# Optimization experiments

Measured on AMD Instinct MI355X. Metric: run time of the kernel, lower is better.

The kernel has to match this reference:

```python
import jax, jax.numpy as jnp
import numpy as np

VOCAB, EMB, OUT = 32000, 1024, 10
B, S = 64, 512

def setup_inputs() -> dict:
    key = jax.random.key(0)
    k1, k2, k3, k4, k5, k6, k7 = jax.random.split(key, 7)
    x = jax.random.randint(k1, (B, S), 0, VOCAB)
    label = jax.random.randint(k2, (B,), 0, OUT)
    emb_table = jax.random.normal(k3, (VOCAB, EMB), dtype=jnp.float32) * 0.02
    W = jax.random.normal(k4, (EMB, EMB), dtype=jnp.float32) / np.sqrt(EMB)
    b = jax.random.normal(k5, (EMB,), dtype=jnp.float32) * 0.01
    Wc = jax.random.normal(k6, (OUT, EMB), dtype=jnp.float32) / np.sqrt(EMB)
    bc = jax.random.normal(k7, (OUT,), dtype=jnp.float32) * 0.01
    return {"x": x, "label": label, "emb_table": emb_table, "W": W, "b": b, "Wc": Wc, "bc": bc}

def reference(x, label, emb_table, W, b, Wc, bc):
    # embedding lookup: (B, S, EMB)
    emb = emb_table[x]
    # affine recurrence h_i = W @ (h_{i-1} + x_i) + b, h_{-1} = 0
    def step(h, xi):
        h = (h + xi) @ W.T + b  # (B, EMB)
        return h, h
    h0 = jnp.zeros((emb.shape[0], emb.shape[2]), dtype=emb.dtype)
    _, hs = jax.lax.scan(step, h0, jnp.swapaxes(emb, 0, 1))  # hs: (S, B, EMB)
    result = jnp.swapaxes(hs, 0, 1)  # (B, S, EMB)
    pred = result @ Wc.T + bc  # (B, S, OUT)
    pred_mean = jnp.mean(pred, axis=1)  # (B, OUT)
    # cross entropy (mean reduction)
    logp = jax.nn.log_softmax(pred_mean, axis=-1)
    loss = -jnp.mean(jnp.take_along_axis(logp, label[:, None], axis=-1))
    return loss
```

## Files before the change

kernel.cpp:

```cpp
#include <hip/hip_runtime.h>

#define OFF_C    0L
#define OFF_CS   11272192L
#define OFF_WP   11354112L
#define OFF_PRED 11446272L
#define OFF_PART 11446912L
#define OFF_U16  11774592L
#define UQAH 0L
#define UQAL 1048576L
#define UQATH 2097152L
#define UQATL 3145728L
#define UQBH 4194304L
#define UQBL 5242880L
#define UQBTH 6291456L
#define UQBTL 7340032L
#define URH  8388608L
#define CSA  1409024L
#define CSB  2621440L

typedef unsigned short u16;
typedef unsigned int u32;
typedef u16 us8 __attribute__((ext_vector_type(8)));
typedef short s8v __attribute__((ext_vector_type(8)));
typedef float f4v __attribute__((ext_vector_type(4)));

__device__ __forceinline__ u16 f2b(float f) {
    u32 u = __float_as_uint(f);
    return (u16)((u + 0x7fffu + ((u >> 16) & 1u)) >> 16);
}
__device__ __forceinline__ float b2f(u16 h) {
    return __uint_as_float((u32)h << 16);
}

__global__ __launch_bounds__(256) void split_w(
    const float* __restrict__ W, u16* __restrict__ Qh, u16* __restrict__ Ql,
    u16* __restrict__ QTh, u16* __restrict__ QTl)
{
    __shared__ u32 T[64][65];
    const int tid = threadIdx.x;
    const int r = tid >> 2, c0 = (tid & 3) << 4;
    alignas(16) u16 h[16], l[16];
    const size_t src = (size_t)(blockIdx.y * 64 + r) * 1024 + blockIdx.x * 64 + c0;
    #pragma unroll
    for (int q = 0; q < 4; q++) {
        float4 v = *(const float4*)(W + src + q * 4);
        float vv[4] = {v.x, v.y, v.z, v.w};
        #pragma unroll
        for (int i = 0; i < 4; i++) {
            u16 hh = f2b(vv[i]);
            u16 ll = f2b(vv[i] - b2f(hh));
            h[q * 4 + i] = hh; l[q * 4 + i] = ll;
            T[c0 + q * 4 + i][r] = ((u32)ll << 16) | hh;
        }
    }
    *(us8*)(Qh + src) = *(const us8*)&h[0];
    *(us8*)(Qh + src + 8) = *(const us8*)&h[8];
    *(us8*)(Ql + src) = *(const us8*)&l[0];
    *(us8*)(Ql + src + 8) = *(const us8*)&l[8];
    __syncthreads();
    alignas(16) u16 th[16], tl[16];
    #pragma unroll
    for (int i = 0; i < 16; i++) {
        u32 v = T[r][c0 + i];
        th[i] = (u16)(v & 0xffffu); tl[i] = (u16)(v >> 16);
    }
    const size_t dst = (size_t)(blockIdx.x * 64 + r) * 1024 + blockIdx.y * 64 + c0;
    *(us8*)(QTh + dst) = *(const us8*)&th[0];
    *(us8*)(QTh + dst + 8) = *(const us8*)&th[8];
    *(us8*)(QTl + dst) = *(const us8*)&tl[0];
    *(us8*)(QTl + dst + 8) = *(const us8*)&tl[8];
}

__global__ __launch_bounds__(256) void d0_k(
    const float* __restrict__ Wc, const float* __restrict__ W, u16* __restrict__ Rh)
{
    __shared__ float WcS[10240];
    __shared__ float red[8][332];
    const int tid = threadIdx.x;
    const int d = tid & 31, kz = tid >> 5;
    const int dbase = blockIdx.x << 5;
    for (int i = tid; i < 2560; i += 256)
        ((float4*)WcS)[i] = ((const float4*)Wc)[i];
    __syncthreads();
    float acc[10] = {};
    const int k0 = kz << 7;
    for (int k = 0; k < 128; k++) {
        float w = W[(size_t)(k0 + k) * 1024 + dbase + d];
        #pragma unroll
        for (int o = 0; o < 10; o++)
            acc[o] = fmaf(WcS[o * 1024 + k0 + k], w, acc[o]);
    }
    #pragma unroll
    for (int o = 0; o < 10; o++) red[kz][o * 32 + d] = acc[o];
    __syncthreads();
    for (int t = tid; t < 320; t += 256) {
        float s = 0.f;
        #pragma unroll
        for (int z = 0; z < 8; z++) s += red[z][t];
        Rh[(size_t)(t >> 5) * 1024 + dbase + (t & 31)] = f2b(s);
    }
}

__global__ __launch_bounds__(256) void gemm_mfma(
    const u16* __restrict__ Ah_g, const u16* __restrict__ Al_g,
    const u16* __restrict__ Rh_g,
    const u16* __restrict__ BTh_g, const u16* __restrict__ BTl_g,
    float* __restrict__ C, int a1M, int a2M, int kc, long cS)
{
    const int M = a1M + a2M;
    __shared__ alignas(16) u16 Ash[4][129][8], Asl[4][129][8];
    __shared__ alignas(16) u16 Bsh[4][129][8], Bsl[4][129][8];
    const int tid = threadIdx.x;
    const int bn = blockIdx.x << 7, bm = blockIdx.y << 7;
    const int kstart = blockIdx.z * kc, kend = kstart + kc;
    const int lane = tid & 63, wid = tid >> 6;
    const int wm = (wid & 1) << 6, wn = (wid >> 1) << 6;
    const int lrow = lane & 15, kq = lane >> 4;
    const int srow = tid >> 1;
    const int skq = (tid & 1) << 1;
    const int sk = skq << 3;

    const u16* pBh = BTh_g + (size_t)(bn + srow) * 1024;
    const u16* pBl = BTl_g + (size_t)(bn + srow) * 1024;

    f4v acc[4][4];
    #pragma unroll
    for (int i = 0; i < 4; i++)
        #pragma unroll
        for (int j = 0; j < 4; j++) acc[i][j] = 0.f;

    if (bm < a1M) {
        const u16* pAh = Ah_g + (size_t)(bm + srow) * 1024;
        const u16* pAl = Al_g + (size_t)(bm + srow) * 1024;
        us8 ah0, ah1, al0, al1, bh0, bh1, bl0, bl1;
        auto loadstep = [&](int k) {
            ah0 = *(const us8*)(pAh + k + sk); ah1 = *(const us8*)(pAh + k + sk + 8);
            al0 = *(const us8*)(pAl + k + sk); al1 = *(const us8*)(pAl + k + sk + 8);
            bh0 = *(const us8*)(pBh + k + sk); bh1 = *(const us8*)(pBh + k + sk + 8);
            bl0 = *(const us8*)(pBl + k + sk); bl1 = *(const us8*)(pBl + k + sk + 8);
        };
        loadstep(kstart);
        for (int k0 = kstart; k0 < kend; k0 += 32) {
            *(us8*)&Ash[skq][srow][0] = ah0;
            *(us8*)&Ash[skq + 1][srow][0] = ah1;
            *(us8*)&Asl[skq][srow][0] = al0;
            *(us8*)&Asl[skq + 1][srow][0] = al1;
            *(us8*)&Bsh[skq][srow][0] = bh0;
            *(us8*)&Bsh[skq + 1][srow][0] = bh1;
            *(us8*)&Bsl[skq][srow][0] = bl0;
            *(us8*)&Bsl[skq + 1][srow][0] = bl1;
            __syncthreads();
            if (k0 + 32 < kend) loadstep(k0 + 32);
            s8v afh[4], afl[4], bfh[4], bfl[4];
            #pragma unroll
            for (int i = 0; i < 4; i++) {
                afh[i] = *(const s8v*)&Ash[kq][wm + (i << 4) + lrow][0];
                afl[i] = *(const s8v*)&Asl[kq][wm + (i << 4) + lrow][0];
                bfh[i] = *(const s8v*)&Bsh[kq][wn + (i << 4) + lrow][0];
                bfl[i] = *(const s8v*)&Bsl[kq][wn + (i << 4) + lrow][0];
            }
            #pragma unroll
            for (int mi = 0; mi < 4; mi++)
                #pragma unroll
                for (int ni = 0; ni < 4; ni++) {
                    acc[mi][ni] = __builtin_amdgcn_mfma_f32_16x16x32_bf16(
                        afh[mi], bfh[ni], acc[mi][ni], 0, 0, 0);
                    acc[mi][ni] = __builtin_amdgcn_mfma_f32_16x16x32_bf16(
                        afl[mi], bfh[ni], acc[mi][ni], 0, 0, 0);
                    acc[mi][ni] = __builtin_amdgcn_mfma_f32_16x16x32_bf16(
                        afh[mi], bfl[ni], acc[mi][ni], 0, 0, 0);
                }
            __syncthreads();
        }
    } else {
        const int rr = bm + srow - a1M;
        const bool aval = (rr < a2M);
        const u16* pAh = Rh_g + (size_t)(aval ? rr : 0) * 1024;
        us8 ah0, ah1, bh0, bh1, bl0, bl1;
        auto loadstep = [&](int k) {
            if (aval) {
                ah0 = *(const us8*)(pAh + k + sk); ah1 = *(const us8*)(pAh + k + sk + 8);
            } else { ah0 = 0; ah1 = 0; }
            bh0 = *(const us8*)(pBh + k + sk); bh1 = *(const us8*)(pBh + k + sk + 8);
            bl0 = *(const us8*)(pBl + k + sk); bl1 = *(const us8*)(pBl + k + sk + 8);
        };
        loadstep(kstart);
        for (int k0 = kstart; k0 < kend; k0 += 32) {
            *(us8*)&Ash[skq][srow][0] = ah0;
            *(us8*)&Ash[skq + 1][srow][0] = ah1;
            *(us8*)&Bsh[skq][srow][0] = bh0;
            *(us8*)&Bsh[skq + 1][srow][0] = bh1;
            *(us8*)&Bsl[skq][srow][0] = bl0;
            *(us8*)&Bsl[skq + 1][srow][0] = bl1;
            __syncthreads();
            if (k0 + 32 < kend) loadstep(k0 + 32);
            s8v afh[4], bfh[4], bfl[4];
            #pragma unroll
            for (int i = 0; i < 4; i++) {
                afh[i] = *(const s8v*)&Ash[kq][wm + (i << 4) + lrow][0];
                bfh[i] = *(const s8v*)&Bsh[kq][wn + (i << 4) + lrow][0];
                bfl[i] = *(const s8v*)&Bsl[kq][wn + (i << 4) + lrow][0];
            }
            #pragma unroll
            for (int mi = 0; mi < 4; mi++)
                #pragma unroll
                for (int ni = 0; ni < 4; ni++) {
                    acc[mi][ni] = __builtin_amdgcn_mfma_f32_16x16x32_bf16(
                        afh[mi], bfh[ni], acc[mi][ni], 0, 0, 0);
                    acc[mi][ni] = __builtin_amdgcn_mfma_f32_16x16x32_bf16(
                        afh[mi], bfl[ni], acc[mi][ni], 0, 0, 0);
                }
            __syncthreads();
        }
    }
    float* Cz = C + (size_t)blockIdx.z * cS;
    #pragma unroll
    for (int mi = 0; mi < 4; mi++)
        #pragma unroll
        for (int i = 0; i < 4; i++) {
            const int gr = bm + wm + (mi << 4) + (kq << 2) + i;
            if (gr >= M) continue;
            #pragma unroll
            for (int ni = 0; ni < 4; ni++)
                Cz[(size_t)gr * 1024 + bn + wn + (ni << 4) + lrow] = acc[mi][ni][i];
        }
}

__global__ __launch_bounds__(256) void combine(
    const float* __restrict__ C, int zsplit, long cS, int a1M, int a2M, int M,
    u16* __restrict__ Qh, u16* __restrict__ Ql,
    u16* __restrict__ QTh, u16* __restrict__ QTl,
    u16* __restrict__ Rh)
{
    __shared__ u32 T[64][65];
    const int tid = threadIdx.x;
    const int r = tid >> 2, c0 = (tid & 3) << 4;
    const int row0 = blockIdx.y << 6, col0 = blockIdx.x << 6;
    const int gr = row0 + r;
    const bool isQ = (row0 < a1M);
    alignas(16) u16 h[16], l[16];
    #pragma unroll
    for (int q = 0; q < 4; q++) {
        float4 v = make_float4(0.f, 0.f, 0.f, 0.f);
        if (gr < M) {
            const float* p = C + (size_t)gr * 1024 + col0 + c0 + q * 4;
            v = *(const float4*)p;
            for (int z = 1; z < zsplit; z++) {
                float4 t2 = *(const float4*)(p + (size_t)z * cS);
                v.x += t2.x; v.y += t2.y; v.z += t2.z; v.w += t2.w;
            }
        }
        float vv[4] = {v.x, v.y, v.z, v.w};
        #pragma unroll
        for (int i = 0; i < 4; i++) {
            u16 hh = f2b(vv[i]);
            u16 ll = f2b(vv[i] - b2f(hh));
            h[q * 4 + i] = hh; l[q * 4 + i] = ll;
            if (isQ) T[c0 + q * 4 + i][r] = ((u32)ll << 16) | hh;
        }
    }
    if (isQ) {
        const size_t dst = (size_t)gr * 1024 + col0 + c0;
        *(us8*)(Qh + dst) = *(const us8*)&h[0];
        *(us8*)(Qh + dst + 8) = *(const us8*)&h[8];
        *(us8*)(Ql + dst) = *(const us8*)&l[0];
        *(us8*)(Ql + dst + 8) = *(const us8*)&l[8];
        __syncthreads();
        alignas(16) u16 th[16], tl[16];
        #pragma unroll
        for (int i = 0; i < 16; i++) {
            u32 v = T[r][c0 + i];
            th[i] = (u16)(v & 0xffffu); tl[i] = (u16)(v >> 16);
        }
        const size_t dt = (size_t)(col0 + r) * 1024 + row0 + c0;
        *(us8*)(QTh + dt) = *(const us8*)&th[0];
        *(us8*)(QTh + dt + 8) = *(const us8*)&th[8];
        *(us8*)(QTl + dt) = *(const us8*)&tl[0];
        *(us8*)(QTl + dt + 8) = *(const us8*)&tl[8];
    } else if (gr < M) {
        const size_t dst = (size_t)(gr - a1M + a2M) * 1024 + col0 + c0;
        *(us8*)(Rh + dst) = *(const us8*)&h[0];
        *(us8*)(Rh + dst + 8) = *(const us8*)&h[8];
    }
}

__global__ __launch_bounds__(256) void prefix_pass1(
    const u16* __restrict__ Rh, float* __restrict__ csum, float* __restrict__ wpart)
{
    const int od = blockIdx.x * 256 + threadIdx.x;
    const int c = blockIdx.y;
    const u16* ph = Rh + (size_t)(c * 64) * 10240 + od;
    float cs = 0.f, wsv = 0.f;
    #pragma unroll 4
    for (int i = 0; i < 64; i++) {
        float v = b2f(ph[(size_t)i * 10240]);
        cs += v;
        wsv += (float)(511 - (c * 64 + i)) * v;
    }
    csum[c * 10240 + od] = cs;
    wpart[c * 10240 + od] = wsv;
}

__global__ __launch_bounds__(256) void prefix_pass2(
    const u16* __restrict__ Rh, const float* __restrict__ csum, float* __restrict__ Acc)
{
    const int od = blockIdx.x * 256 + threadIdx.x;
    const int c = blockIdx.y;
    float run = 0.f;
    #pragma unroll
    for (int c2 = 0; c2 < 8; c2++) {
        float t = csum[c2 * 10240 + od];
        run += (c2 < c) ? t : 0.f;
    }
    const u16* ph = Rh + (size_t)(c * 64) * 10240 + od;
    float* pa = Acc + (size_t)(c * 64) * 10240 + od;
    #pragma unroll 4
    for (int i = 0; i < 64; i++) {
        run += b2f(ph[(size_t)i * 10240]);
        pa[(size_t)i * 10240] = run;
    }
}

__global__ __launch_bounds__(256) void contract_k(
    const float* __restrict__ Acc, const int* __restrict__ x,
    const float* __restrict__ emb, float* __restrict__ part)
{
    __shared__ float As[10240];
    const int tid = threadIdx.x;
    const int j = blockIdx.x;
    const int w = tid >> 6, lane = tid & 63;
    const float4* emb4 = (const float4*)emb;
    float4* As4 = (float4*)As;
    const float4* Ap = (const float4*)(Acc + (size_t)(511 - j) * 10240);

    int i0 = x[((w << 2) + 0) * 512 + j], i1 = x[((w << 2) + 1) * 512 + j];
    int i2 = x[((w << 2) + 2) * 512 + j], i3 = x[((w << 2) + 3) * 512 + j];
    float4 e0[4], e1[4], e2[4], e3[4];
    #pragma unroll
    for (int c = 0; c < 4; c++) {
        e0[c] = emb4[(size_t)i0 * 256 + (c << 6) + lane];
        e1[c] = emb4[(size_t)i1 * 256 + (c << 6) + lane];
        e2[c] = emb4[(size_t)i2 * 256 + (c << 6) + lane];
        e3[c] = emb4[(size_t)i3 * 256 + (c << 6) + lane];
    }
    #pragma unroll
    for (int i = 0; i < 10; i++) As4[tid + (i << 8)] = Ap[tid + (i << 8)];
    __syncthreads();

    for (int chunk = 0; chunk < 4; chunk++) {
        float p0[10], p1[10], p2[10], p3[10];
        #pragma unroll
        for (int o = 0; o < 10; o++) {
            float s0 = 0.f, s1 = 0.f, s2 = 0.f, s3 = 0.f;
            #pragma unroll
            for (int c = 0; c < 4; c++) {
                float4 a = As4[(o << 8) + (c << 6) + lane];
                s0 = fmaf(a.x, e0[c].x, s0); s0 = fmaf(a.y, e0[c].y, s0);
                s0 = fmaf(a.z, e0[c].z, s0); s0 = fmaf(a.w, e0[c].w, s0);
                s1 = fmaf(a.x, e1[c].x, s1); s1 = fmaf(a.y, e1[c].y, s1);
                s1 = fmaf(a.z, e1[c].z, s1); s1 = fmaf(a.w, e1[c].w, s1);
                s2 = fmaf(a.x, e2[c].x, s2); s2 = fmaf(a.y, e2[c].y, s2);
                s2 = fmaf(a.z, e2[c].z, s2); s2 = fmaf(a.w, e2[c].w, s2);
                s3 = fmaf(a.x, e3[c].x, s3); s3 = fmaf(a.y, e3[c].y, s3);
                s3 = fmaf(a.z, e3[c].z, s3); s3 = fmaf(a.w, e3[c].w, s3);
            }
            p0[o] = s0; p1[o] = s1; p2[o] = s2; p3[o] = s3;
        }
        if (chunk < 3) {
            const int bn = ((chunk + 1) << 4) + (w << 2);
            i0 = x[(bn + 0) * 512 + j]; i1 = x[(bn + 1) * 512 + j];
            i2 = x[(bn + 2) * 512 + j]; i3 = x[(bn + 3) * 512 + j];
            #pragma unroll
            for (int c = 0; c < 4; c++) {
                e0[c] = emb4[(size_t)i0 * 256 + (c << 6) + lane];
                e1[c] = emb4[(size_t)i1 * 256 + (c << 6) + lane];
                e2[c] = emb4[(size_t)i2 * 256 + (c << 6) + lane];
                e3[c] = emb4[(size_t)i3 * 256 + (c << 6) + lane];
            }
        }
        #pragma unroll
        for (int o = 0; o < 10; o++) {
            #pragma unroll
            for (int off = 32; off; off >>= 1) {
                p0[o] += __shfl_down(p0[o], off);
                p1[o] += __shfl_down(p1[o], off);
                p2[o] += __shfl_down(p2[o], off);
                p3[o] += __shfl_down(p3[o], off);
            }
        }
        if (lane == 0) {
            const int bbase = (chunk << 4) + (w << 2);
            float* pp = part + (size_t)j * 640 + bbase * 10;
            #pragma unroll
            for (int o = 0; o < 10; o++) {
                pp[o] = p0[o]; pp[10 + o] = p1[o];
                pp[20 + o] = p2[o]; pp[30 + o] = p3[o];
            }
        }
    }
}

__global__ __launch_bounds__(256) void reduce_part(
    const float* __restrict__ part, float* __restrict__ pred)
{
    const int gid = blockIdx.x * 256 + threadIdx.x;
    const int out = gid >> 4, s = gid & 15;
    float p = 0.f;
    #pragma unroll 8
    for (int t = 0; t < 32; t++) p += part[(size_t)(s + (t << 4)) * 640 + out];
    for (int off = 8; off; off >>= 1) p += __shfl_down(p, off, 16);
    if (s == 0) pred[out] = p;
}

__global__ __launch_bounds__(640) void finalize_k(
    const float* __restrict__ pred, const float* __restrict__ wpart,
    const float* __restrict__ Wc, const float* __restrict__ bvec,
    const float* __restrict__ bc, const int* __restrict__ label,
    float* __restrict__ out)
{
    __shared__ float biasv[10];
    const int tid = threadIdx.x;
    {
        int o = tid >> 6, lane = tid & 63;
        float s = 0.f;
        for (int k = lane; k < 1024; k += 64) {
            float wsum = 512.f * Wc[o * 1024 + k];
            #pragma unroll
            for (int c = 0; c < 8; c++) wsum += wpart[c * 10240 + o * 1024 + k];
            s = fmaf(wsum, bvec[k], s);
        }
        for (int off = 32; off; off >>= 1) s += __shfl_down(s, off, 64);
        if (lane == 0) biasv[o] = s;
    }
    __syncthreads();
    if (tid < 64) {
        int b = tid, lab = label[b];
        float v[10], mx = -1e30f;
        #pragma unroll
        for (int o = 0; o < 10; o++) {
            v[o] = (pred[b * 10 + o] + biasv[o]) * (1.f / 512.f) + bc[o];
            mx = fmaxf(mx, v[o]);
        }
        float se = 0.f, vl = 0.f;
        #pragma unroll
        for (int o = 0; o < 10; o++) {
            se += __expf(v[o] - mx);
            if (o == lab) vl = v[o];
        }
        float myloss = (mx + __logf(se)) - vl;
        for (int off = 32; off; off >>= 1) myloss += __shfl_down(myloss, off, 64);
        if (tid == 0) out[0] = myloss * (1.f / 64.f);
    }
}

extern "C" void kernel_launch(void* const* d_in, const int* in_sizes, int n_in,
                              void* d_out, int out_size, void* d_ws, size_t ws_size,
                              hipStream_t stream) {
    const int*   x     = (const int*)d_in[0];
    const int*   label = (const int*)d_in[1];
    const float* emb   = (const float*)d_in[2];
    const float* W     = (const float*)d_in[3];
    const float* bvec  = (const float*)d_in[4];
    const float* Wc    = (const float*)d_in[5];
    const float* bc    = (const float*)d_in[6];
    float* ws    = (float*)d_ws;
    float* C     = ws + OFF_C;
    float* Acc   = ws + OFF_C;
    float* csum  = ws + OFF_CS;
    float* wpart = ws + OFF_WP;
    float* pred  = ws + OFF_PRED;
    float* part  = ws + OFF_PART;
    u16*   ub    = (u16*)(ws + OFF_U16);
    u16* RH = ub + URH;
    u16* qin[4]  = {ub + UQAH, ub + UQAL, ub + UQATH, ub + UQATL};
    u16* qout[4] = {ub + UQBH, ub + UQBL, ub + UQBTH, ub + UQBTL};
    float* out   = (float*)d_out;

    split_w<<<dim3(16, 16), 256, 0, stream>>>(W, qin[0], qin[1], qin[2], qin[3]);
    d0_k<<<32, 256, 0, stream>>>(Wc, W, RH);

    int a2M = 10;
    for (int k = 2; k <= 8; k++) {
        const int a1M = 1024;
        const int M = a1M + a2M;
        const int zs = (M <= 1376) ? 4 : 2;
        const long cS = (zs == 4) ? CSA : CSB;
        const int kc = 1024 / zs;
        dim3 g(8, (M + 127) / 128, zs);
        gemm_mfma<<<g, 256, 0, stream>>>(qin[0], qin[1], RH, qin[2], qin[3],
                                         C, a1M, a2M, kc, cS);
        combine<<<dim3(16, (M + 63) / 64), 256, 0, stream>>>(
            C, zs, cS, a1M, a2M, M,
            qout[0], qout[1], qout[2], qout[3], RH);
        for (int i = 0; i < 4; i++) { u16* t = qin[i]; qin[i] = qout[i]; qout[i] = t; }
        a2M <<= 1;
    }
    for (int e = 0; e < 3; e++) {
        u16* Rin = RH + (size_t)e * 1280 * 1024;
        gemm_mfma<<<dim3(8, 10, 4), 256, 0, stream>>>(
            qin[0], qin[1], Rin, qin[2], qin[3], C, 0, 1280, 256, CSA);
        combine<<<dim3(16, 20), 256, 0, stream>>>(
            C, 4, CSA, 0, 1280, 1280,
            qout[0], qout[1], qout[2], qout[3], Rin);
    }

    prefix_pass1<<<dim3(40, 8), 256, 0, stream>>>(RH, csum, wpart);
    prefix_pass2<<<dim3(40, 8), 256, 0, stream>>>(RH, csum, Acc);
    contract_k<<<512, 256, 0, stream>>>(Acc, x, emb, part);
    reduce_part<<<40, 256, 0, stream>>>(part, pred);
    finalize_k<<<1, 640, 0, stream>>>(pred, wpart, Wc, bvec, bc, label, out);
}
```

Baseline: 518.3 us.

## Merge final power stages into doubling loop and fuse prefix passes

The three fixed 1280-row GEMM+combine rounds become two more doubling iterations. The last one runs a single 2560-row GEMM with no Q squaring, which cuts kernel launches but adds one extra squaring at step 9. The split-K factor is now always 4 with an unrolled combine, and the GEMM gets a min-blocks-per-CU launch bound of 2. The two-pass chunked prefix scan becomes one serial 512-step scan per column that also produces the weighted sum. That removes a launch and the partial buffers but cuts the scan to 40 blocks, which risks low occupancy.

```diff
diff --git a/kernel.cpp b/kernel.cpp
--- a/kernel.cpp
+++ b/kernel.cpp
@@ -101,7 +101,7 @@
     }
 }
 
-__global__ __launch_bounds__(256) void gemm_mfma(
+__global__ __launch_bounds__(256, 2) void gemm_mfma(
     const u16* __restrict__ Ah_g, const u16* __restrict__ Al_g,
     const u16* __restrict__ Rh_g,
     const u16* __restrict__ BTh_g, const u16* __restrict__ BTl_g,
@@ -227,7 +227,7 @@
 }
 
 __global__ __launch_bounds__(256) void combine(
-    const float* __restrict__ C, int zsplit, long cS, int a1M, int a2M, int M,
+    const float* __restrict__ C, long cS, int a1M, int a2M, int M,
     u16* __restrict__ Qh, u16* __restrict__ Ql,
     u16* __restrict__ QTh, u16* __restrict__ QTl,
     u16* __restrict__ Rh)
@@ -245,7 +245,8 @@
         if (gr < M) {
             const float* p = C + (size_t)gr * 1024 + col0 + c0 + q * 4;
             v = *(const float4*)p;
-            for (int z = 1; z < zsplit; z++) {
+            #pragma unroll
+            for (int z = 1; z < 4; z++) {
                 float4 t2 = *(const float4*)(p + (size_t)z * cS);
                 v.x += t2.x; v.y += t2.y; v.z += t2.z; v.w += t2.w;
             }
@@ -284,41 +285,25 @@
     }
 }
 
-__global__ __launch_bounds__(256) void prefix_pass1(
-    const u16* __restrict__ Rh, float* __restrict__ csum, float* __restrict__ wpart)
+__global__ __launch_bounds__(256) void prefix_all(
+    const u16* __restrict__ Rh, float* __restrict__ Acc, float* __restrict__ wfull)
 {
     const int od = blockIdx.x * 256 + threadIdx.x;
-    const int c = blockIdx.y;
-    const u16* ph = Rh + (size_t)(c * 64) * 10240 + od;
-    float cs = 0.f, wsv = 0.f;
-    #pragma unroll 4
-    for (int i = 0; i < 64; i++) {
-        float v = b2f(ph[(size_t)i * 10240]);
-        cs += v;
-        wsv += (float)(511 - (c * 64 + i)) * v;
-    }
-    csum[c * 10240 + od] = cs;
-    wpart[c * 10240 + od] = wsv;
-}
-
-__global__ __launch_bounds__(256) void prefix_pass2(
-    const u16* __restrict__ Rh, const float* __restrict__ csum, float* __restrict__ Acc)
-{
-    const int od = blockIdx.x * 256 + threadIdx.x;
-    const int c = blockIdx.y;
-    float run = 0.f;
-    #pragma unroll
-    for (int c2 = 0; c2 < 8; c2++) {
-        float t = csum[c2 * 10240 + od];
-        run += (c2 < c) ? t : 0.f;
-    }
-    const u16* ph = Rh + (size_t)(c * 64) * 10240 + od;
-    float* pa = Acc + (size_t)(c * 64) * 10240 + od;
-    #pragma unroll 4
-    for (int i = 0; i < 64; i++) {
-        run += b2f(ph[(size_t)i * 10240]);
-        pa[(size_t)i * 10240] = run;
-    }
+    const u16* ph = Rh + od;
+    float* pa = Acc + od;
+    float run = 0.f, wsv = 0.f;
+    for (int m = 0; m < 512; m += 8) {
+        float v[8];
+        #pragma unroll
+        for (int i = 0; i < 8; i++) v[i] = b2f(ph[(size_t)(m + i) * 10240]);
+        #pragma unroll
+        for (int i = 0; i < 8; i++) {
+            run += v[i];
+            wsv += (float)(511 - (m + i)) * v[i];
+            pa[(size_t)(m + i) * 10240] = run;
+        }
+    }
+    wfull[od] = wsv;
 }
 
 __global__ __launch_bounds__(256) void contract_k(
@@ -413,7 +398,7 @@
 }
 
 __global__ __launch_bounds__(640) void finalize_k(
-    const float* __restrict__ pred, const float* __restrict__ wpart,
+    const float* __restrict__ pred, const float* __restrict__ wfull,
     const float* __restrict__ Wc, const float* __restrict__ bvec,
     const float* __restrict__ bc, const int* __restrict__ label,
     float* __restrict__ out)
@@ -424,9 +409,7 @@
         int o = tid >> 6, lane = tid & 63;
         float s = 0.f;
         for (int k = lane; k < 1024; k += 64) {
-            float wsum = 512.f * Wc[o * 1024 + k];
-            #pragma unroll
-            for (int c = 0; c < 8; c++) wsum += wpart[c * 10240 + o * 1024 + k];
+            float wsum = 512.f * Wc[o * 1024 + k] + wfull[o * 1024 + k];
             s = fmaf(wsum, bvec[k], s);
         }
         for (int off = 32; off; off >>= 1) s += __shfl_down(s, off, 64);
@@ -466,8 +449,7 @@
     float* ws    = (float*)d_ws;
     float* C     = ws + OFF_C;
     float* Acc   = ws + OFF_C;
-    float* csum  = ws + OFF_CS;
-    float* wpart = ws + OFF_WP;
+    float* wfull = ws + OFF_WP;
     float* pred  = ws + OFF_PRED;
     float* part  = ws + OFF_PART;
     u16*   ub    = (u16*)(ws + OFF_U16);
@@ -480,33 +462,22 @@
     d0_k<<<32, 256, 0, stream>>>(Wc, W, RH);
 
     int a2M = 10;
-    for (int k = 2; k <= 8; k++) {
-        const int a1M = 1024;
+    for (int k = 2; k <= 10; k++) {
+        const int a1M = (k < 10) ? 1024 : 0;
         const int M = a1M + a2M;
-        const int zs = (M <= 1376) ? 4 : 2;
-        const long cS = (zs == 4) ? CSA : CSB;
-        const int kc = 1024 / zs;
-        dim3 g(8, (M + 127) / 128, zs);
+        const long cS = (M <= 1376) ? CSA : CSB;
+        dim3 g(8, (M + 127) / 128, 4);
         gemm_mfma<<<g, 256, 0, stream>>>(qin[0], qin[1], RH, qin[2], qin[3],
-                                         C, a1M, a2M, kc, cS);
+                                         C, a1M, a2M, 256, cS);
         combine<<<dim3(16, (M + 63) / 64), 256, 0, stream>>>(
-            C, zs, cS, a1M, a2M, M,
+            C, cS, a1M, a2M, M,
             qout[0], qout[1], qout[2], qout[3], RH);
         for (int i = 0; i < 4; i++) { u16* t = qin[i]; qin[i] = qout[i]; qout[i] = t; }
         a2M <<= 1;
     }
-    for (int e = 0; e < 3; e++) {
-        u16* Rin = RH + (size_t)e * 1280 * 1024;
-        gemm_mfma<<<dim3(8, 10, 4), 256, 0, stream>>>(
-            qin[0], qin[1], Rin, qin[2], qin[3], C, 0, 1280, 256, CSA);
-        combine<<<dim3(16, 20), 256, 0, stream>>>(
-            C, 4, CSA, 0, 1280, 1280,
-            qout[0], qout[1], qout[2], qout[3], Rin);
-    }
-
-    prefix_pass1<<<dim3(40, 8), 256, 0, stream>>>(RH, csum, wpart);
-    prefix_pass2<<<dim3(40, 8), 256, 0, stream>>>(RH, csum, Acc);
+
+    prefix_all<<<40, 256, 0, stream>>>(RH, Acc, wfull);
     contract_k<<<512, 256, 0, stream>>>(Acc, x, emb, part);
     reduce_part<<<40, 256, 0, stream>>>(part, pred);
-    finalize_k<<<1, 640, 0, stream>>>(pred, wpart, Wc, bvec, bc, label, out);
-}
+    finalize_k<<<1, 640, 0, stream>>>(pred, wfull, Wc, bvec, bc, label, out);
+}
```

Measured after the change: 533.0 us. 2.8% more time.
